# Kernel optimization log

Measured on AMD Instinct MI355X. Metric: run time of the kernel, lower is better.

Reference implementation:

```python
import jax, jax.numpy as jnp
import numpy as np

CUTOFF = 6.0
PMAX = 256
RBF_DIM = 32
MAX_Z = 90
Z_EMB = 32


def _mlp(x, layers):
    # layers: list of (W, b); SiLU between all but last
    for W, b in layers[:-1]:
        x = jax.nn.silu(x @ W + b)
    W, b = layers[-1]
    return x @ W + b


def _rbf(r):
    centers = jnp.linspace(0.0, CUTOFF, RBF_DIM)
    delta = CUTOFF / (RBF_DIM - 1)
    gamma = 1.0 / (delta * delta + 1e-12)
    return jnp.exp(-gamma * (r[..., None] - centers) ** 2)


def _cutoff_fn(r):
    return 0.5 * (jnp.cos(jnp.pi * r / CUTOFF) + 1.0) * (r <= CUTOFF).astype(r.dtype)


def setup_inputs() -> dict:
    key = jax.random.key(0)
    ks = jax.random.split(key, 24)
    B, N, H, nE, dE = 16, 64, 128, 128, 32
    inp = {
        'h': jax.random.normal(ks[0], (B, N, H), jnp.float32),
        'z': jax.random.randint(ks[1], (B, N), 1, MAX_Z, dtype=jnp.int32).astype(jnp.int64),
        'pos': jax.random.normal(ks[2], (B, N, 3), jnp.float32) * 2.0,
        'mask': jnp.ones((B, N), dtype=bool),
        'e_feat': jax.random.normal(ks[3], (nE, dE), jnp.float32),
    }
    s = 0.05
    # pair-element MLP: in = 2*Z_EMB + dE = 96 -> 128 -> 128 -> 64
    inp['z_emb'] = jax.random.normal(ks[4], (MAX_Z + 1, Z_EMB), jnp.float32) * s
    inp['pw0'] = jax.random.normal(ks[5], (96, 128), jnp.float32) * s
    inp['pb0'] = jnp.zeros((128,), jnp.float32)
    inp['pw1'] = jax.random.normal(ks[6], (128, 128), jnp.float32) * s
    inp['pb1'] = jnp.zeros((128,), jnp.float32)
    inp['pw2'] = jax.random.normal(ks[7], (128, 64), jnp.float32) * s
    inp['pb2'] = jnp.zeros((64,), jnp.float32)
    # geom MLP: in = 2*128 + 3*32 + 1 = 353 -> 256 -> 256 -> 64
    inp['gw0'] = jax.random.normal(ks[8], (353, 256), jnp.float32) * s
    inp['gb0'] = jnp.zeros((256,), jnp.float32)
    inp['gw1'] = jax.random.normal(ks[9], (256, 256), jnp.float32) * s
    inp['gb1'] = jnp.zeros((256,), jnp.float32)
    inp['gw2'] = jax.random.normal(ks[10], (256, 64), jnp.float32) * s
    inp['gb2'] = jnp.zeros((64,), jnp.float32)
    # out proj: 64 -> 256 -> 128
    inp['ow0'] = jax.random.normal(ks[11], (64, 256), jnp.float32) * s
    inp['ob0'] = jnp.zeros((256,), jnp.float32)
    inp['ow1'] = jax.random.normal(ks[12], (256, 128), jnp.float32) * s
    inp['ob1'] = jnp.zeros((128,), jnp.float32)
    return inp


def _forward(h, pos, e_feat, z_emb, pw0, pb0, pw1, pb1, pw2, pb2,
             gw0, gb0, gw1, gb1, gw2, gb2, ow0, ob0, ow1, ob1, z, mask):
    B, N, H = h.shape
    # absorber-relative geometry (absorber_index = 0)
    rel = pos - pos[:, 0:1, :]                     # [B,N,3]
    r = jnp.linalg.norm(rel, axis=-1)              # [B,N]
    valid = mask & (jnp.arange(N) != 0)[None, :] & (r <= CUTOFF)
    # vectorized triplet-path enumeration: all j<k pairs, sort by score, keep PMAX
    jU, kU = np.triu_indices(N, k=1)               # [M]
    jU = jnp.asarray(jU); kU = jnp.asarray(kU)
    pair_valid = valid[:, jU] & valid[:, kU]       # [B,M]
    r0j_all = r[:, jU]
    r0k_all = r[:, kU]
    rjk_all = jnp.linalg.norm(pos[:, kU] - pos[:, jU], axis=-1)
    score = r0j_all + r0k_all + 0.5 * rjk_all
    score = jnp.where(pair_valid, score, jnp.inf)
    order = jnp.argsort(score, axis=1)[:, :PMAX]   # [B,PMAX]
    pmask = jnp.take_along_axis(pair_valid, order, axis=1)
    j_idx = jnp.where(pmask, jU[order], 0)         # [B,PMAX]
    k_idx = jnp.where(pmask, kU[order], 0)
    # gather features / positions
    hj = jnp.take_along_axis(h, j_idx[:, :, None], axis=1)     # [B,P,H]
    hk = jnp.take_along_axis(h, k_idx[:, :, None], axis=1)
    posj = jnp.take_along_axis(pos, j_idx[:, :, None], axis=1)  # [B,P,3]
    posk = jnp.take_along_axis(pos, k_idx[:, :, None], axis=1)
    pos0 = pos[:, 0:1, :]
    vj = posj - pos0
    vk = posk - pos0
    vjk = posk - posj
    r0j = jnp.linalg.norm(vj, axis=-1)
    r0k = jnp.linalg.norm(vk, axis=-1)
    rjk = jnp.linalg.norm(vjk, axis=-1)
    uj = vj / jnp.maximum(r0j[..., None], 1e-8)
    uk = vk / jnp.maximum(r0k[..., None], 1e-8)
    cosang = jnp.clip(jnp.sum(uj * uk, axis=-1, keepdims=True), -1.0, 1.0)
    f0j = _rbf(jnp.minimum(r0j, CUTOFF))
    f0k = _rbf(jnp.minimum(r0k, CUTOFF))
    fjk = _rbf(jnp.minimum(rjk, CUTOFF))
    geom_in = jnp.concatenate([hj, hk, f0j, f0k, fjk, cosang], axis=-1)  # [B,P,353]
    g_geom = _mlp(geom_in, [(gw0, gb0), (gw1, gb1), (gw2, gb2)])         # [B,P,S]
    # pair-element energy scattering
    P = PMAX
    nE, dE = e_feat.shape
    zj = jnp.take_along_axis(z, j_idx, axis=1)
    zk = jnp.take_along_axis(z, k_idx, axis=1)
    ej = jnp.broadcast_to(z_emb[zj][:, :, None, :], (B, P, nE, Z_EMB))
    ek = jnp.broadcast_to(z_emb[zk][:, :, None, :], (B, P, nE, Z_EMB))
    ef = jnp.broadcast_to(e_feat[None, None, :, :], (B, P, nE, dE))
    pe_in = jnp.concatenate([ej, ek, ef], axis=-1)                       # [B,P,nE,96]
    g_elem = _mlp(pe_in, [(pw0, pb0), (pw1, pb1), (pw2, pb2)])           # [B,P,nE,S]
    # cutoff weighting + masked mean over paths
    cw = _cutoff_fn(r0j) * _cutoff_fn(r0k) * _cutoff_fn(rjk)             # [B,P]
    w = cw * pmask.astype(cw.dtype)                                      # [B,P]
    contrib = g_geom[:, :, None, :] * g_elem * w[:, :, None, None]
    agg = contrib.sum(axis=1)                                            # [B,nE,S]
    norm = jnp.maximum(w.sum(axis=1), 1e-8)[:, None, None]               # [B,1,1]
    agg = agg / norm
    return _mlp(agg, [(ow0, ob0), (ow1, ob1)])                           # [B,nE,out]


def reference(h, z, pos, mask, e_feat, z_emb, pw0, pb0, pw1, pb1, pw2, pb2,
              gw0, gb0, gw1, gb1, gw2, gb2, ow0, ob0, ow1, ob1):
    return _forward(h, pos, e_feat, z_emb, pw0, pb0, pw1, pb1, pw2, pb2,
                    gw0, gb0, gw1, gb1, gw2, gb2, ow0, ob0, ow1, ob1, z, mask)
```

## Files before the change

### kernel.cpp

```cpp
#include <hip/hip_runtime.h>
#include <math.h>

#define NB 16
#define NA 64
#define NHD 128
#define NPAIR 2016
#define PSEL 256
#define NEL 128
#define WS_FLAG   0
#define WS_SUMW   1024
#define WS_SELJ   2048
#define WS_SELK   (WS_SELJ + 16384)
#define WS_SCAL   (WS_SELK + 16384)
#define WS_AE     (WS_SCAL + 131072)
#define WS_GG     (WS_AE + 65536)
#define WS_A0     (WS_GG + 1048576)
#define WS_AGG    (WS_A0 + 2097152)
#define WS_W1F    (WS_AGG + 524288)
#define WS_W2F    (WS_W1F + 32768)
#define WS_G0F    (WS_W2F + 16384)
#define WS_G1F    (WS_G0F + 196608)
#define WS_G2F    (WS_G1F + 131072)

typedef short v8s __attribute__((ext_vector_type(8)));
typedef float v4f __attribute__((ext_vector_type(4)));

__device__ __forceinline__ float siluf_fast(float x) {
  float e = __expf(-x);
  return x * __builtin_amdgcn_rcpf(1.0f + e);
}
__device__ __forceinline__ unsigned short f2bf(float f) {
  unsigned int u = __float_as_uint(f);
  return (unsigned short)((u + 0x7fffu + ((u >> 16) & 1u)) >> 16);
}
__device__ __forceinline__ unsigned int pk_bf16(float fa, float fb) {
  unsigned int ua = __float_as_uint(fa), ub = __float_as_uint(fb);
  ua = ua + 0x7fffu + ((ua >> 16) & 1u);
  ub = ub + 0x7fffu + ((ub >> 16) & 1u);
  return __builtin_amdgcn_perm(ub, ua, 0x07060302u);
}
__device__ __forceinline__ float cutf(float r) {
  return (r <= 6.0f) ? (0.5f * (cosf((3.14159265358979323846f * r) / 6.0f) + 1.0f)) : 0.0f;
}
__device__ __forceinline__ float rbff(float r, int i) {
  float rc = fminf(r, 6.0f);
  float c = (float)i * (6.0f / 31.0f);
  float d = rc - c;
  return expf(-26.694445f * d * d);
}
__device__ __forceinline__ void pair_jk(int p, int& j, int& k) {
  int jj = (int)((127.0 - sqrt(16129.0 - 8.0 * (double)p)) * 0.5);
  if (jj < 0) jj = 0;
  if (jj > 62) jj = 62;
  while (jj < 62 && (63 * (jj + 1) - ((jj + 1) * jj) / 2) <= p) jj++;
  while (jj > 0 && (63 * jj - (jj * (jj - 1)) / 2) > p) jj--;
  j = jj;
  k = p - (63 * jj - (jj * (jj - 1)) / 2) + jj + 1;
}

__global__ __launch_bounds__(256) void k_prep(
    const int* __restrict__ z, const float* __restrict__ ef,
    const float* __restrict__ pw0, const float* __restrict__ pw1,
    const float* __restrict__ pw2, const float* __restrict__ gw0,
    const float* __restrict__ gw1, const float* __restrict__ gw2, char* ws) {
  int idx = blockIdx.x * 256 + threadIdx.x;
  if (idx == 0) *((int*)(ws + WS_FLAG)) = (z[1] == 0) ? 1 : 0;
  if (idx < 16384) {
    int j = idx & 7, l = (idx >> 3) & 63, t2 = idx >> 9;
    int kk = t2 & 3, nt = t2 >> 2;
    int n = 16 * nt + (l & 15), k = 32 * kk + (l >> 4) * 8 + j;
    ((unsigned short*)(ws + WS_W1F))[idx] = f2bf(pw1[k * 128 + n]);
  } else if (idx < 24576) {
    int id = idx - 16384;
    int j = id & 7, l = (id >> 3) & 63, t2 = id >> 9;
    int kk = t2 & 3, nt = t2 >> 2;
    int n = 16 * nt + (l & 15), k = 32 * kk + (l >> 4) * 8 + j;
    ((unsigned short*)(ws + WS_W2F))[id] = f2bf(pw2[k * 64 + n]);
  } else if (idx < 122880) {
    int id = idx - 24576;
    int j = id & 7, l = (id >> 3) & 63, t2 = id >> 9;
    int kk = t2 % 12, nt = t2 / 12;
    int n = 16 * nt + (l & 15), k = 32 * kk + (l >> 4) * 8 + j;
    float v = (k < 353) ? gw0[k * 256 + n] : 0.0f;
    ((unsigned short*)(ws + WS_G0F))[id] = f2bf(v);
  } else if (idx < 188416) {
    int id = idx - 122880;
    int j = id & 7, l = (id >> 3) & 63, t2 = id >> 9;
    int kk = t2 & 7, nt = t2 >> 3;
    int n = 16 * nt + (l & 15), k = 32 * kk + (l >> 4) * 8 + j;
    ((unsigned short*)(ws + WS_G1F))[id] = f2bf(gw1[k * 256 + n]);
  } else if (idx < 204800) {
    int id = idx - 188416;
    int j = id & 7, l = (id >> 3) & 63, t2 = id >> 9;
    int kk = t2 & 7, nt = t2 >> 3;
    int n = 16 * nt + (l & 15), k = 32 * kk + (l >> 4) * 8 + j;
    ((unsigned short*)(ws + WS_G2F))[id] = f2bf(gw2[k * 64 + n]);
  } else if (idx < 221184) {
    int id = idx - 204800;
    int e = id >> 7, d = id & 127;
    float a = 0.0f;
    for (int i = 0; i < 32; i++) a += ef[e * 32 + i] * pw0[(64 + i) * 128 + d];
    ((float*)(ws + WS_AE))[e * 128 + d] = a;
  }
}

__global__ __launch_bounds__(256) void k1_select(const float* __restrict__ pos, char* ws) {
#pragma clang fp contract(off)
  int b = blockIdx.x, t = threadIdx.x;
  __shared__ float px[64], py[64], pz[64], rr[64];
  __shared__ int hist[256], scan[256];
  __shared__ unsigned long long selk[256];
  __shared__ float wred[256];
  __shared__ unsigned long long s_pref, s_kstar;
  __shared__ int s_K, s_done, s_digit, s_exc, s_cnt;
  if (t < 64) {
    px[t] = pos[(b * 64 + t) * 3 + 0];
    py[t] = pos[(b * 64 + t) * 3 + 1];
    pz[t] = pos[(b * 64 + t) * 3 + 2];
  }
  if (t == 0) { s_pref = 0; s_K = PSEL; s_done = 0; s_cnt = 0; }
  __syncthreads();
  if (t < 64) {
    float dx = px[t] - px[0], dy = py[t] - py[0], dz = pz[t] - pz[0];
    rr[t] = sqrtf((dx * dx + dy * dy) + dz * dz);
  }
  __syncthreads();
  unsigned long long keys[8];
#pragma unroll
  for (int ii = 0; ii < 8; ii++) {
    int p = t + 256 * ii;
    unsigned long long key = 0xFFFFFFFFFFFFFFFFull;
    if (p < NPAIR) {
      int j, k;
      pair_jk(p, j, k);
      bool vj = (j != 0) && (rr[j] <= 6.0f);
      bool vk = (rr[k] <= 6.0f);
      unsigned int sb = 0x7f800000u;
      if (vj && vk) {
        float dx = px[k] - px[j], dy = py[k] - py[j], dz = pz[k] - pz[j];
        float rjk = sqrtf((dx * dx + dy * dy) + dz * dz);
        float score = (rr[j] + rr[k]) + 0.5f * rjk;
        sb = __float_as_uint(score);
      }
      key = (((unsigned long long)sb) << 32) | (unsigned int)p;
    }
    keys[ii] = key;
  }
  for (int shift = 56; shift >= 0; shift -= 8) {
    if (s_done) break;
    hist[t] = 0;
    __syncthreads();
    unsigned long long hiMask = (shift == 56) ? 0ull : (~0ull << (shift + 8));
    unsigned long long pref = s_pref;
    int K = s_K;
#pragma unroll
    for (int ii = 0; ii < 8; ii++) {
      if ((keys[ii] & hiMask) == pref)
        atomicAdd(&hist[(int)((keys[ii] >> shift) & 255)], 1);
    }
    __syncthreads();
    scan[t] = hist[t];
    __syncthreads();
    for (int off = 1; off < 256; off <<= 1) {
      int add = (t >= off) ? scan[t - off] : 0;
      __syncthreads();
      scan[t] += add;
      __syncthreads();
    }
    int inc = scan[t], exc = inc - hist[t];
    if (exc < K && K <= inc) { s_digit = t; s_exc = exc; }
    __syncthreads();
    int d = s_digit, exc2 = s_exc, cnt = hist[d];
    unsigned long long npref = pref | ((unsigned long long)d << shift);
    if (cnt == 1) {
      unsigned long long inclMask = hiMask | (255ull << shift);
#pragma unroll
      for (int ii = 0; ii < 8; ii++)
        if ((keys[ii] & inclMask) == npref) s_kstar = keys[ii];
      if (t == 0) s_done = 1;
    } else if (shift == 0) {
      if (t == 0) { s_kstar = npref; s_done = 1; }
    } else {
      if (t == 0) { s_pref = npref; s_K = K - exc2; }
    }
    __syncthreads();
  }
  unsigned long long kstar = s_kstar;
#pragma unroll
  for (int ii = 0; ii < 8; ii++) {
    if (keys[ii] <= kstar) {
      int slot = atomicAdd(&s_cnt, 1);
      selk[slot] = keys[ii];
    }
  }
  __syncthreads();
  float myw = 0.0f;
  {
    unsigned long long key = selk[t];
    unsigned int sb = (unsigned int)(key >> 32);
    int p = (int)(key & 0xFFFFFFFFu);
    bool pv = (sb < 0x7f800000u);
    int j = 0, k = 0;
    if (pv) pair_jk(p, j, k);
    float r0j = rr[j], r0k = rr[k];
    float vjx = px[j] - px[0], vjy = py[j] - py[0], vjz = pz[j] - pz[0];
    float vkx = px[k] - px[0], vky = py[k] - py[0], vkz = pz[k] - pz[0];
    float dx = px[k] - px[j], dy = py[k] - py[j], dz = pz[k] - pz[j];
    float rjk = sqrtf((dx * dx + dy * dy) + dz * dz);
    float ij = 1.0f / fmaxf(r0j, 1e-8f);
    float ik = 1.0f / fmaxf(r0k, 1e-8f);
    float cs = (vjx * vkx + vjy * vky + vjz * vkz) * ij * ik;
    cs = fminf(1.0f, fmaxf(-1.0f, cs));
    float w = pv ? (cutf(r0j) * cutf(r0k) * cutf(rjk)) : 0.0f;
    int* selJ = (int*)(ws + WS_SELJ);
    int* selK = (int*)(ws + WS_SELK);
    float* scal = (float*)(ws + WS_SCAL);
    selJ[b * PSEL + t] = j;
    selK[b * PSEL + t] = k;
    float* s = &scal[(b * PSEL + t) * 8];
    s[0] = r0j; s[1] = r0k; s[2] = rjk; s[3] = cs; s[4] = w;
    myw = w;
  }
  wred[t] = myw;
  __syncthreads();
  for (int s2 = 128; s2 > 0; s2 >>= 1) {
    if (t < s2) wred[t] += wred[t + s2];
    __syncthreads();
  }
  if (t == 0) ((float*)(ws + WS_SUMW))[b] = fmaxf(wred[0], 1e-8f);
}

__global__ __launch_bounds__(128) void k2b_a0(const int* __restrict__ z,
                                              const float* __restrict__ zemb,
                                              const float* __restrict__ pw0,
                                              const float* __restrict__ pb0, char* ws) {
  int p = blockIdx.x, b = blockIdx.y, d = threadIdx.x;
  const int* selJ = (const int*)(ws + WS_SELJ);
  const int* selK = (const int*)(ws + WS_SELK);
  int is64 = *((const int*)(ws + WS_FLAG));
  float* A0 = (float*)(ws + WS_A0);
  int j = selJ[b * PSEL + p], k = selK[b * PSEL + p];
  __shared__ float zr[64];
  if (d < 64) {
    int atom = (d < 32) ? j : k;
    int zi = b * 64 + atom;
    int zv = is64 ? z[zi * 2] : z[zi];
    zr[d] = zemb[zv * 32 + (d & 31)];
  }
  __syncthreads();
  float a = pb0[d];
  for (int i = 0; i < 32; i++) {
    a += zr[i] * pw0[i * 128 + d];
    a += zr[32 + i] * pw0[(32 + i) * 128 + d];
  }
  A0[(b * PSEL + p) * 128 + d] = a;
}

#define LP3 392
#define LQ3 264
__global__ __launch_bounds__(256) void k3_geom(const float* __restrict__ h,
    const float* __restrict__ gb0, const float* __restrict__ gb1,
    const float* __restrict__ gb2, char* ws) {
  int blk = blockIdx.x;
  int b = blk >> 4, p0 = (blk & 15) * 16;
  int t = threadIdx.x;
  int lane = t & 63, w = t >> 6;
  int q = lane >> 4, m4 = lane & 15;
  const int* selJ = (const int*)(ws + WS_SELJ);
  const int* selK = (const int*)(ws + WS_SELK);
  const float* scal = (const float*)(ws + WS_SCAL);
  const float* sumw = (const float*)(ws + WS_SUMW);
  float* gg = (float*)(ws + WS_GG);
  const unsigned short* G0F = (const unsigned short*)(ws + WS_G0F);
  const unsigned short* G1F = (const unsigned short*)(ws + WS_G1F);
  const unsigned short* G2F = (const unsigned short*)(ws + WS_G2F);
  __shared__ __align__(16) unsigned short xs[16 * LP3];
  __shared__ __align__(16) unsigned short x1s[16 * LQ3];
  __shared__ __align__(16) unsigned short x2s[16 * LQ3];
  const v4f z4 = {0.f, 0.f, 0.f, 0.f};
  {
    int row = t & 15, fs = t >> 4;
    int p = p0 + row;
    int j = selJ[b * PSEL + p], k = selK[b * PSEL + p];
    const float* s = &scal[(b * PSEL + p) * 8];
    float r0j = s[0], r0k = s[1], rjk = s[2], cs = s[3];
    for (int f = fs; f < 384; f += 16) {
      float v;
      if (f < 128) v = h[(b * 64 + j) * 128 + f];
      else if (f < 256) v = h[(b * 64 + k) * 128 + (f - 128)];
      else if (f < 288) v = rbff(r0j, f - 256);
      else if (f < 320) v = rbff(r0k, f - 288);
      else if (f < 352) v = rbff(rjk, f - 320);
      else if (f == 352) v = cs;
      else v = 0.0f;
      xs[row * LP3 + f] = f2bf(v);
    }
  }
  __syncthreads();
  {
    v4f acc[4];
#pragma unroll
    for (int nt = 0; nt < 4; nt++) acc[nt] = z4;
    for (int kk = 0; kk < 12; kk++) {
      v8s bf = *(const v8s*)&xs[m4 * LP3 + 32 * kk + 8 * q];
#pragma unroll
      for (int nt = 0; nt < 4; nt++) {
        v8s wf = *(const v8s*)&G0F[(((4 * w + nt) * 12 + kk) * 64 + lane) * 8];
        acc[nt] = __builtin_amdgcn_mfma_f32_16x16x32_bf16(wf, bf, acc[nt], 0, 0, 0);
      }
    }
#pragma unroll
    for (int nt = 0; nt < 4; nt++) {
      int n0 = 64 * w + 16 * nt + 4 * q;
      float4 bias = *(const float4*)&gb0[n0];
      uint2 o;
      o.x = pk_bf16(siluf_fast(acc[nt][0] + bias.x), siluf_fast(acc[nt][1] + bias.y));
      o.y = pk_bf16(siluf_fast(acc[nt][2] + bias.z), siluf_fast(acc[nt][3] + bias.w));
      *(uint2*)&x1s[m4 * LQ3 + n0] = o;
    }
  }
  __syncthreads();
  {
    v4f acc[4];
#pragma unroll
    for (int nt = 0; nt < 4; nt++) acc[nt] = z4;
    for (int kk = 0; kk < 8; kk++) {
      v8s bf = *(const v8s*)&x1s[m4 * LQ3 + 32 * kk + 8 * q];
#pragma unroll
      for (int nt = 0; nt < 4; nt++) {
        v8s wf = *(const v8s*)&G1F[(((4 * w + nt) * 8 + kk) * 64 + lane) * 8];
        acc[nt] = __builtin_amdgcn_mfma_f32_16x16x32_bf16(wf, bf, acc[nt], 0, 0, 0);
      }
    }
#pragma unroll
    for (int nt = 0; nt < 4; nt++) {
      int n0 = 64 * w + 16 * nt + 4 * q;
      float4 bias = *(const float4*)&gb1[n0];
      uint2 o;
      o.x = pk_bf16(siluf_fast(acc[nt][0] + bias.x), siluf_fast(acc[nt][1] + bias.y));
      o.y = pk_bf16(siluf_fast(acc[nt][2] + bias.z), siluf_fast(acc[nt][3] + bias.w));
      *(uint2*)&x2s[m4 * LQ3 + n0] = o;
    }
  }
  __syncthreads();
  {
    v4f acc = z4;
    for (int kk = 0; kk < 8; kk++) {
      v8s bf = *(const v8s*)&x2s[m4 * LQ3 + 32 * kk + 8 * q];
      v8s wf = *(const v8s*)&G2F[((w * 8 + kk) * 64 + lane) * 8];
      acc = __builtin_amdgcn_mfma_f32_16x16x32_bf16(wf, bf, acc, 0, 0, 0);
    }
    int p = p0 + m4;
    float wp = scal[(b * PSEL + p) * 8 + 4];
    float s2 = wp / sumw[b];
    int n0 = 16 * w + 4 * q;
    float4 bias = *(const float4*)&gb2[n0];
    float4 o;
    o.x = (acc[0] + bias.x) * s2;
    o.y = (acc[1] + bias.y) * s2;
    o.z = (acc[2] + bias.z) * s2;
    o.w = (acc[3] + bias.w) * s2;
    *(float4*)&gg[(b * PSEL + p) * 64 + n0] = o;
  }
}

#define LP 136
__global__ __launch_bounds__(256, 4) void k4_elem(
    const float* __restrict__ pb1, const float* __restrict__ pb2, char* ws) {
  int et = blockIdx.x, b = blockIdx.y, pc = blockIdx.z;
  int t = threadIdx.x;
  int lane = t & 63, w = t >> 6;
  int q = lane >> 4, m4 = lane & 15;
  const float* A0 = (const float*)(ws + WS_A0);
  const float* Ae = (const float*)(ws + WS_AE);
  const float* gg = (const float*)(ws + WS_GG);
  const unsigned short* W1F = (const unsigned short*)(ws + WS_W1F);
  const unsigned short* W2F = (const unsigned short*)(ws + WS_W2F);
  float* agg = (float*)(ws + WS_AGG);
  __shared__ __align__(16) unsigned short x0s[64 * LP];
  __shared__ __align__(16) unsigned short x1s[64 * LP];
  int e0 = et * 8;

  v8s w1f[2][4], w2f[4];
#pragma unroll
  for (int ct = 0; ct < 2; ct++)
#pragma unroll
    for (int kk = 0; kk < 4; kk++)
      w1f[ct][kk] = *(const v8s*)&W1F[(((2 * w + ct) * 4 + kk) * 64 + lane) * 8];
#pragma unroll
  for (int kk = 0; kk < 4; kk++)
    w2f[kk] = *(const v8s*)&W2F[(((w) * 4 + kk) * 64 + lane) * 8];
  float4 b1v[2];
  b1v[0] = *(const float4*)&pb1[32 * w + 4 * q];
  b1v[1] = *(const float4*)&pb1[32 * w + 16 + 4 * q];
  float4 b2v = *(const float4*)&pb2[16 * w + 4 * q];

  int pl = t >> 5, k0 = (t & 31) * 4;
  const float* a0p = A0 + (b * PSEL + pc * 64 + pl) * 128 + k0;
  const float* aep = Ae + e0 * 128 + k0;
  unsigned short* xw = &x0s[pl * LP + k0];
  const float* ggp = gg + (b * PSEL + pc * 64 + (lane & 7)) * 64 + 16 * w + 4 * q;

  v4f aggR[4];
  const v4f z4 = {0.f, 0.f, 0.f, 0.f};
#pragma unroll
  for (int mt = 0; mt < 4; mt++) aggR[mt] = z4;

  for (int g2 = 0; g2 < 8; g2++) {
    float4 a0v = *(const float4*)a0p;
#pragma unroll
    for (int it = 0; it < 8; it++) {
      float4 aev = *(const float4*)(aep + it * 128);
      uint2 o;
      o.x = pk_bf16(siluf_fast(a0v.x + aev.x), siluf_fast(a0v.y + aev.y));
      o.y = pk_bf16(siluf_fast(a0v.z + aev.z), siluf_fast(a0v.w + aev.w));
      *(uint2*)(xw + it * 8 * LP) = o;
    }
    a0p += 1024;
    __syncthreads();
    v4f acc1[4][2];
#pragma unroll
    for (int mt = 0; mt < 4; mt++) { acc1[mt][0] = z4; acc1[mt][1] = z4; }
#pragma unroll
    for (int kk = 0; kk < 4; kk++) {
#pragma unroll
      for (int mt = 0; mt < 4; mt++) {
        v8s bf = *(const v8s*)&x0s[(16 * mt + m4) * LP + 32 * kk + 8 * q];
        acc1[mt][0] = __builtin_amdgcn_mfma_f32_16x16x32_bf16(w1f[0][kk], bf, acc1[mt][0], 0, 0, 0);
        acc1[mt][1] = __builtin_amdgcn_mfma_f32_16x16x32_bf16(w1f[1][kk], bf, acc1[mt][1], 0, 0, 0);
      }
    }
#pragma unroll
    for (int mt = 0; mt < 4; mt++) {
#pragma unroll
      for (int ct = 0; ct < 2; ct++) {
        float4 bias = b1v[ct];
        uint2 o;
        o.x = pk_bf16(siluf_fast(acc1[mt][ct][0] + bias.x), siluf_fast(acc1[mt][ct][1] + bias.y));
        o.y = pk_bf16(siluf_fast(acc1[mt][ct][2] + bias.z), siluf_fast(acc1[mt][ct][3] + bias.w));
        int n0 = 32 * w + 16 * ct + 4 * q;
        *(uint2*)&x1s[(16 * mt + m4) * LP + n0] = o;
      }
    }
    __syncthreads();
    v4f acc2[4];
#pragma unroll
    for (int mt = 0; mt < 4; mt++) acc2[mt] = z4;
#pragma unroll
    for (int kk = 0; kk < 4; kk++) {
#pragma unroll
      for (int mt = 0; mt < 4; mt++) {
        v8s bf = *(const v8s*)&x1s[(16 * mt + m4) * LP + 32 * kk + 8 * q];
        acc2[mt] = __builtin_amdgcn_mfma_f32_16x16x32_bf16(w2f[kk], bf, acc2[mt], 0, 0, 0);
      }
    }
    float4 gv = *(const float4*)ggp;
    ggp += 512;
#pragma unroll
    for (int mt = 0; mt < 4; mt++) {
      aggR[mt][0] += gv.x * (acc2[mt][0] + b2v.x);
      aggR[mt][1] += gv.y * (acc2[mt][1] + b2v.y);
      aggR[mt][2] += gv.z * (acc2[mt][2] + b2v.z);
      aggR[mt][3] += gv.w * (acc2[mt][3] + b2v.w);
    }
  }
#pragma unroll
  for (int mt = 0; mt < 4; mt++) {
#pragma unroll
    for (int r = 0; r < 4; r++) {
      float v = aggR[mt][r];
      v += __shfl_xor(v, 1);
      v += __shfl_xor(v, 2);
      v += __shfl_xor(v, 4);
      if ((lane & 7) == 0) {
        int e = 2 * mt + ((lane >> 3) & 1);
        int n = 16 * w + 4 * q + r;
        atomicAdd(&agg[(b * NEL + e0 + e) * 64 + n], v);
      }
    }
  }
}

__global__ __launch_bounds__(256) void k5_out(
    const float* __restrict__ ow0, const float* __restrict__ ob0,
    const float* __restrict__ ow1, const float* __restrict__ ob1,
    const char* ws, float* __restrict__ out) {
  int row0 = blockIdx.x * 16;
  int t = threadIdx.x;
  const float* agg = (const float*)(ws + WS_AGG);
  __shared__ float xT[64][16];
  __shared__ float x1T[256][16];
  {
    int row = t & 15, fs = t >> 4;
    for (int f = fs; f < 64; f += 16) xT[f][row] = agg[(row0 + row) * 64 + f];
  }
  __syncthreads();
  {
    int r0 = (t & 3) * 4, c0 = (t >> 2) * 4;
    float acc[4][4] = {};
    for (int k2 = 0; k2 < 64; k2++) {
      float4 xv = *(const float4*)&xT[k2][r0];
      float4 wv = *(const float4*)&ow0[k2 * 256 + c0];
      float xs2[4] = {xv.x, xv.y, xv.z, xv.w};
      float wss[4] = {wv.x, wv.y, wv.z, wv.w};
#pragma unroll
      for (int i = 0; i < 4; i++)
#pragma unroll
        for (int j2 = 0; j2 < 4; j2++) acc[i][j2] += xs2[i] * wss[j2];
    }
#pragma unroll
    for (int jj = 0; jj < 4; jj++) {
      float bias = ob0[c0 + jj];
#pragma unroll
      for (int i = 0; i < 4; i++) x1T[c0 + jj][r0 + i] = siluf_fast(acc[i][jj] + bias);
    }
  }
  __syncthreads();
  {
    int r0 = (t & 3) * 4, c0 = (t >> 2) * 2;
    float acc[4][2] = {};
    for (int k2 = 0; k2 < 256; k2++) {
      float4 xv = *(const float4*)&x1T[k2][r0];
      float2 wv = *(const float2*)&ow1[k2 * 128 + c0];
      float xs2[4] = {xv.x, xv.y, xv.z, xv.w};
#pragma unroll
      for (int i = 0; i < 4; i++) {
        acc[i][0] += xs2[i] * wv.x;
        acc[i][1] += xs2[i] * wv.y;
      }
    }
#pragma unroll
    for (int i = 0; i < 4; i++)
#pragma unroll
      for (int j2 = 0; j2 < 2; j2++)
        out[(row0 + r0 + i) * 128 + c0 + j2] = acc[i][j2] + ob1[c0 + j2];
  }
}

extern "C" void kernel_launch(void* const* d_in, const int* in_sizes, int n_in,
                              void* d_out, int out_size, void* d_ws, size_t ws_size,
                              hipStream_t stream) {
  const float* h     = (const float*)d_in[0];
  const int*   z     = (const int*)d_in[1];
  const float* pos   = (const float*)d_in[2];
  const float* efeat = (const float*)d_in[4];
  const float* zemb  = (const float*)d_in[5];
  const float* pw0 = (const float*)d_in[6];
  const float* pb0 = (const float*)d_in[7];
  const float* pw1 = (const float*)d_in[8];
  const float* pb1 = (const float*)d_in[9];
  const float* pw2 = (const float*)d_in[10];
  const float* pb2 = (const float*)d_in[11];
  const float* gw0 = (const float*)d_in[12];
  const float* gb0 = (const float*)d_in[13];
  const float* gw1 = (const float*)d_in[14];
  const float* gb1 = (const float*)d_in[15];
  const float* gw2 = (const float*)d_in[16];
  const float* gb2 = (const float*)d_in[17];
  const float* ow0 = (const float*)d_in[18];
  const float* ob0 = (const float*)d_in[19];
  const float* ow1 = (const float*)d_in[20];
  const float* ob1 = (const float*)d_in[21];
  char* ws = (char*)d_ws;
  float* out = (float*)d_out;

  hipMemsetAsync(ws + WS_AGG, 0, NB * NEL * 64 * sizeof(float), stream);
  k_prep<<<864, 256, 0, stream>>>(z, efeat, pw0, pw1, pw2, gw0, gw1, gw2, ws);
  k1_select<<<16, 256, 0, stream>>>(pos, ws);
  k2b_a0<<<dim3(256, 16), 128, 0, stream>>>(z, zemb, pw0, pb0, ws);
  k3_geom<<<256, 256, 0, stream>>>(h, gb0, gb1, gb2, ws);
  k4_elem<<<dim3(16, 16, 4), 256, 0, stream>>>(pb1, pb2, ws);
  k5_out<<<128, 256, 0, stream>>>(ow0, ob0, ow1, ob1, ws, out);
}
```

Baseline: 229.6 us.

## Precompute per-element z-embedding projections and merge prep, select, memset kernels

The first-layer z-embedding projection is now computed per atomic number, as lookup tables of 91x128 entries for the j and k slots, instead of per selected pair. k4 gathers these rows by z index, so the per-pair A0 buffer and the k2b_a0 kernel go away. The weight prep, pair selection and AGG zeroing are merged into one launch, with separate block ranges for prep work and the 16 selection blocks, which removes the memset and two kernel launches. The pb0 bias is folded into the Ae table. The cost is extra gathers in k4 plus the prep and selection work sharing a single grid.

```diff
diff --git a/kernel.cpp b/kernel.cpp
--- a/kernel.cpp
+++ b/kernel.cpp
@@ -3,24 +3,34 @@
 
 #define NB 16
 #define NA 64
-#define NHD 128
 #define NPAIR 2016
 #define PSEL 256
 #define NEL 128
-#define WS_FLAG   0
-#define WS_SUMW   1024
+#define WS_SUMW   0
 #define WS_SELJ   2048
 #define WS_SELK   (WS_SELJ + 16384)
 #define WS_SCAL   (WS_SELK + 16384)
 #define WS_AE     (WS_SCAL + 131072)
 #define WS_GG     (WS_AE + 65536)
-#define WS_A0     (WS_GG + 1048576)
-#define WS_AGG    (WS_A0 + 2097152)
+#define WS_ZRJ    (WS_GG + 1048576)
+#define WS_ZRK    (WS_ZRJ + 47104)
+#define WS_AGG    (WS_ZRK + 47104)
 #define WS_W1F    (WS_AGG + 524288)
 #define WS_W2F    (WS_W1F + 32768)
 #define WS_G0F    (WS_W2F + 16384)
 #define WS_G1F    (WS_G0F + 196608)
 #define WS_G2F    (WS_G1F + 131072)
+
+#define PREP_BLOCKS 1467
+#define IDX_W1F  16384
+#define IDX_W2F  24576
+#define IDX_G0F  122880
+#define IDX_G1F  188416
+#define IDX_G2F  204800
+#define IDX_AE   221184
+#define IDX_ZRJ  232832
+#define IDX_ZRK  244480
+#define IDX_AGG  375552
 
 typedef short v8s __attribute__((ext_vector_type(8)));
 typedef float v4f __attribute__((ext_vector_type(4)));
@@ -58,202 +68,200 @@
   k = p - (63 * jj - (jj * (jj - 1)) / 2) + jj + 1;
 }
 
-__global__ __launch_bounds__(256) void k_prep(
+__global__ __launch_bounds__(256) void kA(
     const int* __restrict__ z, const float* __restrict__ ef,
-    const float* __restrict__ pw0, const float* __restrict__ pw1,
-    const float* __restrict__ pw2, const float* __restrict__ gw0,
-    const float* __restrict__ gw1, const float* __restrict__ gw2, char* ws) {
-  int idx = blockIdx.x * 256 + threadIdx.x;
-  if (idx == 0) *((int*)(ws + WS_FLAG)) = (z[1] == 0) ? 1 : 0;
-  if (idx < 16384) {
-    int j = idx & 7, l = (idx >> 3) & 63, t2 = idx >> 9;
-    int kk = t2 & 3, nt = t2 >> 2;
-    int n = 16 * nt + (l & 15), k = 32 * kk + (l >> 4) * 8 + j;
-    ((unsigned short*)(ws + WS_W1F))[idx] = f2bf(pw1[k * 128 + n]);
-  } else if (idx < 24576) {
-    int id = idx - 16384;
-    int j = id & 7, l = (id >> 3) & 63, t2 = id >> 9;
-    int kk = t2 & 3, nt = t2 >> 2;
-    int n = 16 * nt + (l & 15), k = 32 * kk + (l >> 4) * 8 + j;
-    ((unsigned short*)(ws + WS_W2F))[id] = f2bf(pw2[k * 64 + n]);
-  } else if (idx < 122880) {
-    int id = idx - 24576;
-    int j = id & 7, l = (id >> 3) & 63, t2 = id >> 9;
-    int kk = t2 % 12, nt = t2 / 12;
-    int n = 16 * nt + (l & 15), k = 32 * kk + (l >> 4) * 8 + j;
-    float v = (k < 353) ? gw0[k * 256 + n] : 0.0f;
-    ((unsigned short*)(ws + WS_G0F))[id] = f2bf(v);
-  } else if (idx < 188416) {
-    int id = idx - 122880;
-    int j = id & 7, l = (id >> 3) & 63, t2 = id >> 9;
-    int kk = t2 & 7, nt = t2 >> 3;
-    int n = 16 * nt + (l & 15), k = 32 * kk + (l >> 4) * 8 + j;
-    ((unsigned short*)(ws + WS_G1F))[id] = f2bf(gw1[k * 256 + n]);
-  } else if (idx < 204800) {
-    int id = idx - 188416;
-    int j = id & 7, l = (id >> 3) & 63, t2 = id >> 9;
-    int kk = t2 & 7, nt = t2 >> 3;
-    int n = 16 * nt + (l & 15), k = 32 * kk + (l >> 4) * 8 + j;
-    ((unsigned short*)(ws + WS_G2F))[id] = f2bf(gw2[k * 64 + n]);
-  } else if (idx < 221184) {
-    int id = idx - 204800;
-    int e = id >> 7, d = id & 127;
-    float a = 0.0f;
-    for (int i = 0; i < 32; i++) a += ef[e * 32 + i] * pw0[(64 + i) * 128 + d];
-    ((float*)(ws + WS_AE))[e * 128 + d] = a;
-  }
-}
-
-__global__ __launch_bounds__(256) void k1_select(const float* __restrict__ pos, char* ws) {
-#pragma clang fp contract(off)
-  int b = blockIdx.x, t = threadIdx.x;
+    const float* __restrict__ pos,
+    const float* __restrict__ pw0, const float* __restrict__ pb0,
+    const float* __restrict__ pw1, const float* __restrict__ pw2,
+    const float* __restrict__ gw0, const float* __restrict__ gw1,
+    const float* __restrict__ gw2, const float* __restrict__ zemb, char* ws) {
   __shared__ float px[64], py[64], pz[64], rr[64];
   __shared__ int hist[256], scan[256];
   __shared__ unsigned long long selk[256];
   __shared__ float wred[256];
   __shared__ unsigned long long s_pref, s_kstar;
   __shared__ int s_K, s_done, s_digit, s_exc, s_cnt;
-  if (t < 64) {
-    px[t] = pos[(b * 64 + t) * 3 + 0];
-    py[t] = pos[(b * 64 + t) * 3 + 1];
-    pz[t] = pos[(b * 64 + t) * 3 + 2];
-  }
-  if (t == 0) { s_pref = 0; s_K = PSEL; s_done = 0; s_cnt = 0; }
-  __syncthreads();
-  if (t < 64) {
-    float dx = px[t] - px[0], dy = py[t] - py[0], dz = pz[t] - pz[0];
-    rr[t] = sqrtf((dx * dx + dy * dy) + dz * dz);
-  }
-  __syncthreads();
-  unsigned long long keys[8];
-#pragma unroll
-  for (int ii = 0; ii < 8; ii++) {
-    int p = t + 256 * ii;
-    unsigned long long key = 0xFFFFFFFFFFFFFFFFull;
-    if (p < NPAIR) {
-      int j, k;
-      pair_jk(p, j, k);
-      bool vj = (j != 0) && (rr[j] <= 6.0f);
-      bool vk = (rr[k] <= 6.0f);
-      unsigned int sb = 0x7f800000u;
-      if (vj && vk) {
-        float dx = px[k] - px[j], dy = py[k] - py[j], dz = pz[k] - pz[j];
-        float rjk = sqrtf((dx * dx + dy * dy) + dz * dz);
-        float score = (rr[j] + rr[k]) + 0.5f * rjk;
-        sb = __float_as_uint(score);
-      }
-      key = (((unsigned long long)sb) << 32) | (unsigned int)p;
-    }
-    keys[ii] = key;
-  }
-  for (int shift = 56; shift >= 0; shift -= 8) {
-    if (s_done) break;
-    hist[t] = 0;
+  int blk = blockIdx.x, t = threadIdx.x;
+
+  if (blk < PREP_BLOCKS) {
+    int idx = blk * 256 + t;
+    if (idx < IDX_W1F) {
+      int j = idx & 7, l = (idx >> 3) & 63, t2 = idx >> 9;
+      int kk = t2 & 3, nt = t2 >> 2;
+      int n = 16 * nt + (l & 15), k = 32 * kk + (l >> 4) * 8 + j;
+      ((unsigned short*)(ws + WS_W1F))[idx] = f2bf(pw1[k * 128 + n]);
+    } else if (idx < IDX_W2F) {
+      int id = idx - IDX_W1F;
+      int j = id & 7, l = (id >> 3) & 63, t2 = id >> 9;
+      int kk = t2 & 3, nt = t2 >> 2;
+      int n = 16 * nt + (l & 15), k = 32 * kk + (l >> 4) * 8 + j;
+      ((unsigned short*)(ws + WS_W2F))[id] = f2bf(pw2[k * 64 + n]);
+    } else if (idx < IDX_G0F) {
+      int id = idx - IDX_W2F;
+      int j = id & 7, l = (id >> 3) & 63, t2 = id >> 9;
+      int kk = t2 % 12, nt = t2 / 12;
+      int n = 16 * nt + (l & 15), k = 32 * kk + (l >> 4) * 8 + j;
+      float v = (k < 353) ? gw0[k * 256 + n] : 0.0f;
+      ((unsigned short*)(ws + WS_G0F))[id] = f2bf(v);
+    } else if (idx < IDX_G1F) {
+      int id = idx - IDX_G0F;
+      int j = id & 7, l = (id >> 3) & 63, t2 = id >> 9;
+      int kk = t2 & 7, nt = t2 >> 3;
+      int n = 16 * nt + (l & 15), k = 32 * kk + (l >> 4) * 8 + j;
+      ((unsigned short*)(ws + WS_G1F))[id] = f2bf(gw1[k * 256 + n]);
+    } else if (idx < IDX_G2F) {
+      int id = idx - IDX_G1F;
+      int j = id & 7, l = (id >> 3) & 63, t2 = id >> 9;
+      int kk = t2 & 7, nt = t2 >> 3;
+      int n = 16 * nt + (l & 15), k = 32 * kk + (l >> 4) * 8 + j;
+      ((unsigned short*)(ws + WS_G2F))[id] = f2bf(gw2[k * 64 + n]);
+    } else if (idx < IDX_AE) {
+      int id = idx - IDX_G2F;
+      int e = id >> 7, d = id & 127;
+      float a = pb0[d];
+      for (int i = 0; i < 32; i++) a += ef[e * 32 + i] * pw0[(64 + i) * 128 + d];
+      ((float*)(ws + WS_AE))[e * 128 + d] = a;
+    } else if (idx < IDX_ZRJ) {
+      int id = idx - IDX_AE;
+      int zv = id >> 7, d = id & 127;
+      float a = 0.0f;
+      for (int i = 0; i < 32; i++) a += zemb[zv * 32 + i] * pw0[i * 128 + d];
+      ((float*)(ws + WS_ZRJ))[id] = a;
+    } else if (idx < IDX_ZRK) {
+      int id = idx - IDX_ZRJ;
+      int zv = id >> 7, d = id & 127;
+      float a = 0.0f;
+      for (int i = 0; i < 32; i++) a += zemb[zv * 32 + i] * pw0[(32 + i) * 128 + d];
+      ((float*)(ws + WS_ZRK))[id] = a;
+    } else if (idx < IDX_AGG) {
+      ((float*)(ws + WS_AGG))[idx - IDX_ZRK] = 0.0f;
+    }
+    return;
+  }
+
+  {
+#pragma clang fp contract(off)
+    int b = blk - PREP_BLOCKS;
+    int is64 = (z[1] == 0) ? 1 : 0;
+    if (t < 64) {
+      px[t] = pos[(b * 64 + t) * 3 + 0];
+      py[t] = pos[(b * 64 + t) * 3 + 1];
+      pz[t] = pos[(b * 64 + t) * 3 + 2];
+    }
+    if (t == 0) { s_pref = 0; s_K = PSEL; s_done = 0; s_cnt = 0; }
     __syncthreads();
-    unsigned long long hiMask = (shift == 56) ? 0ull : (~0ull << (shift + 8));
-    unsigned long long pref = s_pref;
-    int K = s_K;
+    if (t < 64) {
+      float dx = px[t] - px[0], dy = py[t] - py[0], dz = pz[t] - pz[0];
+      rr[t] = sqrtf((dx * dx + dy * dy) + dz * dz);
+    }
+    __syncthreads();
+    unsigned long long keys[8];
 #pragma unroll
     for (int ii = 0; ii < 8; ii++) {
-      if ((keys[ii] & hiMask) == pref)
-        atomicAdd(&hist[(int)((keys[ii] >> shift) & 255)], 1);
+      int p = t + 256 * ii;
+      unsigned long long key = 0xFFFFFFFFFFFFFFFFull;
+      if (p < NPAIR) {
+        int j, k;
+        pair_jk(p, j, k);
+        bool vj = (j != 0) && (rr[j] <= 6.0f);
+        bool vk = (rr[k] <= 6.0f);
+        unsigned int sb = 0x7f800000u;
+        if (vj && vk) {
+          float dx = px[k] - px[j], dy = py[k] - py[j], dz = pz[k] - pz[j];
+          float rjk = sqrtf((dx * dx + dy * dy) + dz * dz);
+          float score = (rr[j] + rr[k]) + 0.5f * rjk;
+          sb = __float_as_uint(score);
+        }
+        key = (((unsigned long long)sb) << 32) | (unsigned int)p;
+      }
+      keys[ii] = key;
+    }
+    for (int shift = 56; shift >= 0; shift -= 8) {
+      if (s_done) break;
+      hist[t] = 0;
+      __syncthreads();
+      unsigned long long hiMask = (shift == 56) ? 0ull : (~0ull << (shift + 8));
+      unsigned long long pref = s_pref;
+      int K = s_K;
+#pragma unroll
+      for (int ii = 0; ii < 8; ii++) {
+        if ((keys[ii] & hiMask) == pref)
+          atomicAdd(&hist[(int)((keys[ii] >> shift) & 255)], 1);
+      }
+      __syncthreads();
+      scan[t] = hist[t];
+      __syncthreads();
+      for (int off = 1; off < 256; off <<= 1) {
+        int add = (t >= off) ? scan[t - off] : 0;
+        __syncthreads();
+        scan[t] += add;
+        __syncthreads();
+      }
+      int inc = scan[t], exc = inc - hist[t];
+      if (exc < K && K <= inc) { s_digit = t; s_exc = exc; }
+      __syncthreads();
+      int d = s_digit, exc2 = s_exc, cnt = hist[d];
+      unsigned long long npref = pref | ((unsigned long long)d << shift);
+      if (cnt == 1) {
+        unsigned long long inclMask = hiMask | (255ull << shift);
+#pragma unroll
+        for (int ii = 0; ii < 8; ii++)
+          if ((keys[ii] & inclMask) == npref) s_kstar = keys[ii];
+        if (t == 0) s_done = 1;
+      } else if (shift == 0) {
+        if (t == 0) { s_kstar = npref; s_done = 1; }
+      } else {
+        if (t == 0) { s_pref = npref; s_K = K - exc2; }
+      }
+      __syncthreads();
+    }
+    unsigned long long kstar = s_kstar;
+#pragma unroll
+    for (int ii = 0; ii < 8; ii++) {
+      if (keys[ii] <= kstar) {
+        int slot = atomicAdd(&s_cnt, 1);
+        selk[slot] = keys[ii];
+      }
     }
     __syncthreads();
-    scan[t] = hist[t];
+    float myw = 0.0f;
+    {
+      unsigned long long key = selk[t];
+      unsigned int sb = (unsigned int)(key >> 32);
+      int p = (int)(key & 0xFFFFFFFFu);
+      bool pv = (sb < 0x7f800000u);
+      int j = 0, k = 0;
+      if (pv) pair_jk(p, j, k);
+      float r0j = rr[j], r0k = rr[k];
+      float vjx = px[j] - px[0], vjy = py[j] - py[0], vjz = pz[j] - pz[0];
+      float vkx = px[k] - px[0], vky = py[k] - py[0], vkz = pz[k] - pz[0];
+      float dx = px[k] - px[j], dy = py[k] - py[j], dz = pz[k] - pz[j];
+      float rjk = sqrtf((dx * dx + dy * dy) + dz * dz);
+      float ij = 1.0f / fmaxf(r0j, 1e-8f);
+      float ik = 1.0f / fmaxf(r0k, 1e-8f);
+      float cs = (vjx * vkx + vjy * vky + vjz * vkz) * ij * ik;
+      cs = fminf(1.0f, fmaxf(-1.0f, cs));
+      float w = pv ? (cutf(r0j) * cutf(r0k) * cutf(rjk)) : 0.0f;
+      int zj = is64 ? z[(b * 64 + j) * 2] : z[b * 64 + j];
+      int zk = is64 ? z[(b * 64 + k) * 2] : z[b * 64 + k];
+      int* selJ = (int*)(ws + WS_SELJ);
+      int* selK = (int*)(ws + WS_SELK);
+      float* scal = (float*)(ws + WS_SCAL);
+      selJ[b * PSEL + t] = j;
+      selK[b * PSEL + t] = k;
+      float* s = &scal[(b * PSEL + t) * 8];
+      s[0] = r0j; s[1] = r0k; s[2] = rjk; s[3] = cs; s[4] = w;
+      ((int*)s)[5] = zj; ((int*)s)[6] = zk;
+      myw = w;
+    }
+    wred[t] = myw;
     __syncthreads();
-    for (int off = 1; off < 256; off <<= 1) {
-      int add = (t >= off) ? scan[t - off] : 0;
+    for (int s2 = 128; s2 > 0; s2 >>= 1) {
+      if (t < s2) wred[t] += wred[t + s2];
       __syncthreads();
-      scan[t] += add;
-      __syncthreads();
-    }
-    int inc = scan[t], exc = inc - hist[t];
-    if (exc < K && K <= inc) { s_digit = t; s_exc = exc; }
-    __syncthreads();
-    int d = s_digit, exc2 = s_exc, cnt = hist[d];
-    unsigned long long npref = pref | ((unsigned long long)d << shift);
-    if (cnt == 1) {
-      unsigned long long inclMask = hiMask | (255ull << shift);
-#pragma unroll
-      for (int ii = 0; ii < 8; ii++)
-        if ((keys[ii] & inclMask) == npref) s_kstar = keys[ii];
-      if (t == 0) s_done = 1;
-    } else if (shift == 0) {
-      if (t == 0) { s_kstar = npref; s_done = 1; }
-    } else {
-      if (t == 0) { s_pref = npref; s_K = K - exc2; }
-    }
-    __syncthreads();
-  }
-  unsigned long long kstar = s_kstar;
-#pragma unroll
-  for (int ii = 0; ii < 8; ii++) {
-    if (keys[ii] <= kstar) {
-      int slot = atomicAdd(&s_cnt, 1);
-      selk[slot] = keys[ii];
-    }
-  }
-  __syncthreads();
-  float myw = 0.0f;
-  {
-    unsigned long long key = selk[t];
-    unsigned int sb = (unsigned int)(key >> 32);
-    int p = (int)(key & 0xFFFFFFFFu);
-    bool pv = (sb < 0x7f800000u);
-    int j = 0, k = 0;
-    if (pv) pair_jk(p, j, k);
-    float r0j = rr[j], r0k = rr[k];
-    float vjx = px[j] - px[0], vjy = py[j] - py[0], vjz = pz[j] - pz[0];
-    float vkx = px[k] - px[0], vky = py[k] - py[0], vkz = pz[k] - pz[0];
-    float dx = px[k] - px[j], dy = py[k] - py[j], dz = pz[k] - pz[j];
-    float rjk = sqrtf((dx * dx + dy * dy) + dz * dz);
-    float ij = 1.0f / fmaxf(r0j, 1e-8f);
-    float ik = 1.0f / fmaxf(r0k, 1e-8f);
-    float cs = (vjx * vkx + vjy * vky + vjz * vkz) * ij * ik;
-    cs = fminf(1.0f, fmaxf(-1.0f, cs));
-    float w = pv ? (cutf(r0j) * cutf(r0k) * cutf(rjk)) : 0.0f;
-    int* selJ = (int*)(ws + WS_SELJ);
-    int* selK = (int*)(ws + WS_SELK);
-    float* scal = (float*)(ws + WS_SCAL);
-    selJ[b * PSEL + t] = j;
-    selK[b * PSEL + t] = k;
-    float* s = &scal[(b * PSEL + t) * 8];
-    s[0] = r0j; s[1] = r0k; s[2] = rjk; s[3] = cs; s[4] = w;
-    myw = w;
-  }
-  wred[t] = myw;
-  __syncthreads();
-  for (int s2 = 128; s2 > 0; s2 >>= 1) {
-    if (t < s2) wred[t] += wred[t + s2];
-    __syncthreads();
-  }
-  if (t == 0) ((float*)(ws + WS_SUMW))[b] = fmaxf(wred[0], 1e-8f);
-}
-
-__global__ __launch_bounds__(128) void k2b_a0(const int* __restrict__ z,
-                                              const float* __restrict__ zemb,
-                                              const float* __restrict__ pw0,
-                                              const float* __restrict__ pb0, char* ws) {
-  int p = blockIdx.x, b = blockIdx.y, d = threadIdx.x;
-  const int* selJ = (const int*)(ws + WS_SELJ);
-  const int* selK = (const int*)(ws + WS_SELK);
-  int is64 = *((const int*)(ws + WS_FLAG));
-  float* A0 = (float*)(ws + WS_A0);
-  int j = selJ[b * PSEL + p], k = selK[b * PSEL + p];
-  __shared__ float zr[64];
-  if (d < 64) {
-    int atom = (d < 32) ? j : k;
-    int zi = b * 64 + atom;
-    int zv = is64 ? z[zi * 2] : z[zi];
-    zr[d] = zemb[zv * 32 + (d & 31)];
-  }
-  __syncthreads();
-  float a = pb0[d];
-  for (int i = 0; i < 32; i++) {
-    a += zr[i] * pw0[i * 128 + d];
-    a += zr[32 + i] * pw0[(32 + i) * 128 + d];
-  }
-  A0[(b * PSEL + p) * 128 + d] = a;
+    }
+    if (t == 0) ((float*)(ws + WS_SUMW))[b] = fmaxf(wred[0], 1e-8f);
+  }
 }
 
 #define LP3 392
@@ -371,9 +379,10 @@
   int t = threadIdx.x;
   int lane = t & 63, w = t >> 6;
   int q = lane >> 4, m4 = lane & 15;
-  const float* A0 = (const float*)(ws + WS_A0);
   const float* Ae = (const float*)(ws + WS_AE);
   const float* gg = (const float*)(ws + WS_GG);
+  const float* zrJ = (const float*)(ws + WS_ZRJ);
+  const float* zrK = (const float*)(ws + WS_ZRK);
   const unsigned short* W1F = (const unsigned short*)(ws + WS_W1F);
   const unsigned short* W2F = (const unsigned short*)(ws + WS_W2F);
   float* agg = (float*)(ws + WS_AGG);
@@ -396,7 +405,7 @@
   float4 b2v = *(const float4*)&pb2[16 * w + 4 * q];
 
   int pl = t >> 5, k0 = (t & 31) * 4;
-  const float* a0p = A0 + (b * PSEL + pc * 64 + pl) * 128 + k0;
+  const int* sI = (const int*)(ws + WS_SCAL) + (b * PSEL + pc * 64 + pl) * 8;
   const float* aep = Ae + e0 * 128 + k0;
   unsigned short* xw = &x0s[pl * LP + k0];
   const float* ggp = gg + (b * PSEL + pc * 64 + (lane & 7)) * 64 + 16 * w + 4 * q;
@@ -407,7 +416,13 @@
   for (int mt = 0; mt < 4; mt++) aggR[mt] = z4;
 
   for (int g2 = 0; g2 < 8; g2++) {
-    float4 a0v = *(const float4*)a0p;
+    int zj = sI[5], zk = sI[6];
+    sI += 64;
+    float4 aj = *(const float4*)&zrJ[zj * 128 + k0];
+    float4 ak = *(const float4*)&zrK[zk * 128 + k0];
+    float4 a0v;
+    a0v.x = aj.x + ak.x; a0v.y = aj.y + ak.y;
+    a0v.z = aj.z + ak.z; a0v.w = aj.w + ak.w;
 #pragma unroll
     for (int it = 0; it < 8; it++) {
       float4 aev = *(const float4*)(aep + it * 128);
@@ -416,7 +431,6 @@
       o.y = pk_bf16(siluf_fast(a0v.z + aev.z), siluf_fast(a0v.w + aev.w));
       *(uint2*)(xw + it * 8 * LP) = o;
     }
-    a0p += 1024;
     __syncthreads();
     v4f acc1[4][2];
 #pragma unroll
@@ -564,10 +578,8 @@
   char* ws = (char*)d_ws;
   float* out = (float*)d_out;
 
-  hipMemsetAsync(ws + WS_AGG, 0, NB * NEL * 64 * sizeof(float), stream);
-  k_prep<<<864, 256, 0, stream>>>(z, efeat, pw0, pw1, pw2, gw0, gw1, gw2, ws);
-  k1_select<<<16, 256, 0, stream>>>(pos, ws);
-  k2b_a0<<<dim3(256, 16), 128, 0, stream>>>(z, zemb, pw0, pb0, ws);
+  kA<<<PREP_BLOCKS + 16, 256, 0, stream>>>(z, efeat, pos, pw0, pb0, pw1, pw2,
+                                           gw0, gw1, gw2, zemb, ws);
   k3_geom<<<256, 256, 0, stream>>>(h, gb0, gb1, gb2, ws);
   k4_elem<<<dim3(16, 16, 4), 256, 0, stream>>>(pb1, pb2, ws);
   k5_out<<<128, 256, 0, stream>>>(ow0, ob0, ow1, ob1, ws, out);
```

Measured after the change: 216.0 us. -5.9%, faster.
